# Kernel optimization log

Measured on AMD Instinct MI355X. Metric: run time of the kernel, lower is better.

The kernel has to match this reference:

```python
import jax, jax.numpy as jnp
import numpy as np

B, T, IN, H, OUT = 64, 2048, 64, 512, 32


def setup_inputs() -> dict:
    key = jax.random.key(0)
    ks = jax.random.split(key, 8)
    # xavier_normal with gain=0.5: std = gain * sqrt(2/(fan_in+fan_out))
    std_fz = 0.5 * np.sqrt(2.0 / ((IN + H) + 2 * H))
    std_r = 0.5 * np.sqrt(2.0 / ((IN + H) + H))
    # nn.Linear default init: uniform(-1/sqrt(fan_in), 1/sqrt(fan_in))
    lim = 1.0 / np.sqrt(H)
    return {
        "u": jax.random.normal(ks[0], (B, T, IN), dtype=jnp.float32),
        "x0": jax.random.uniform(ks[1], (B, 1, H), dtype=jnp.float32),
        "kernel_fz": std_fz * jax.random.normal(ks[2], (IN + H, 2 * H), dtype=jnp.float32),
        "bias_fz": jnp.zeros((2 * H,), dtype=jnp.float32),
        "kernel_r": std_r * jax.random.normal(ks[3], (IN + H, H), dtype=jnp.float32),
        "bias_r": jnp.zeros((H,), dtype=jnp.float32),
        "W_out": jax.random.uniform(ks[4], (OUT, H), dtype=jnp.float32, minval=-lim, maxval=lim),
        "b_out": jax.random.uniform(ks[5], (OUT,), dtype=jnp.float32, minval=-lim, maxval=lim),
    }


def reference(u, x0, kernel_fz, bias_fz, kernel_r, bias_r, W_out, b_out):
    Hd = kernel_r.shape[1]
    x_init = x0[:, 0, :]  # [B, H]

    def step(x, u_t):
        # u_t: [B, IN], x: [B, H]
        fz = jax.nn.sigmoid(jnp.concatenate([u_t, x], axis=-1) @ kernel_fz + bias_fz)
        f, z = fz[:, :Hd], fz[:, Hd:]
        r = jnp.tanh(jnp.concatenate([u_t, f * x], axis=-1) @ kernel_r + bias_r)
        xk = (1.0 - z) * x + z * r
        y = x @ W_out.T + b_out  # output computed from PREVIOUS state, as in torch step()
        return xk, y

    u_tb = jnp.swapaxes(u, 0, 1)  # [T, B, IN]
    _, ys = jax.lax.scan(step, x_init, u_tb)  # ys: [T, B, OUT]
    return jnp.swapaxes(ys, 0, 1)  # [B, T, OUT]
```

## Files before the change

kernel.cpp:

```cpp
#include <hip/hip_runtime.h>
#include <stdint.h>

#define B_    64
#define T_    2048
#define IN_   64
#define H_    512
#define H2_   1024
#define OUT_  32
#define KTOT  576

#define NBG   8
#define NCG   32
#define NTHR  256
#define BPG   8
#define KSL   18
#define RS    12

#define ABORT_IDX   0
#define CTR_OFF     1024
#define CTR_STRIDE  1024
#define NCTR        (NBG * 2)
#define BUF_BASE    (CTR_OFF + NCTR * CTR_STRIDE)
#define XSLAB       32768

__device__ __forceinline__ void gpubf(float* p, float v) {
  asm volatile("global_atomic_swap %0, %1, off sc1\n\ts_waitcnt vmcnt(0)"
               :: "v"(p), "v"(v) : "memory");
}
__device__ __forceinline__ void gaddu(unsigned* p, unsigned v) {
  asm volatile("global_atomic_add %0, %1, off sc1"
               :: "v"(p), "v"(v) : "memory");
}
__device__ __forceinline__ unsigned gpollu(const unsigned* p) {
  unsigned v;
  asm volatile("global_load_dword %0, %1, off sc0 sc1\n\ts_waitcnt vmcnt(0)"
               : "=v"(v) : "v"(p) : "memory");
  return v;
}
__device__ __forceinline__ void gload4x4(const float* p0, const float* p1,
                                         const float* p2, const float* p3,
                                         float4& a, float4& b, float4& c, float4& d) {
  asm volatile(
      "global_load_dwordx4 %0, %4, off sc0 sc1\n\t"
      "global_load_dwordx4 %1, %5, off sc0 sc1\n\t"
      "global_load_dwordx4 %2, %6, off sc0 sc1\n\t"
      "global_load_dwordx4 %3, %7, off sc0 sc1\n\t"
      "s_waitcnt vmcnt(0)"
      : "=&v"(a), "=&v"(b), "=&v"(c), "=&v"(d)
      : "v"(p0), "v"(p1), "v"(p2), "v"(p3)
      : "memory");
}

__global__ __launch_bounds__(256) void gru_init(float* ws, const float* __restrict__ x0) {
  int i = blockIdx.x * blockDim.x + threadIdx.x;
  int stride = gridDim.x * blockDim.x;
  unsigned* w = (unsigned*)ws;
  for (int k = i; k < BUF_BASE; k += stride) w[k] = 0u;
  for (int k = i; k < NBG * H_ * BPG; k += stride) {
    int bg = k >> 12, j = (k >> 3) & (H_ - 1), b = k & 7;
    ws[BUF_BASE + k] = x0[(bg * 8 + b) * H_ + j];
  }
}

__device__ __forceinline__ void gbar_arrive(unsigned* ctr) {
  __syncthreads();
  if (threadIdx.x == 0) gaddu(ctr, 1u);
}

__device__ __forceinline__ bool gbar_wait(unsigned* ctr, unsigned target,
                                          unsigned* abort_w) {
  __shared__ int s_ok;
  if (threadIdx.x == 0) {
    int ok = 1;
    int polls = 0;
    while (gpollu(ctr) < target) {
      __builtin_amdgcn_s_sleep(1);
      if ((++polls & 255) == 0) {
        if (__hip_atomic_load(abort_w, __ATOMIC_RELAXED, __HIP_MEMORY_SCOPE_AGENT) != 0u ||
            polls > 2000000) {
          __hip_atomic_store(abort_w, 1u, __ATOMIC_RELAXED, __HIP_MEMORY_SCOPE_AGENT);
          ok = 0;
          break;
        }
      }
    }
    s_ok = ok;
  }
  __syncthreads();
  __atomic_signal_fence(__ATOMIC_ACQUIRE);
  return s_ok != 0;
}

__global__ __launch_bounds__(NTHR, 1) void gru_main(
    const float* __restrict__ u, const float* __restrict__ kfz,
    const float* __restrict__ bfz, const float* __restrict__ kr,
    const float* __restrict__ br, const float* __restrict__ wout,
    const float* __restrict__ bout, float* __restrict__ out, float* ws) {
  unsigned* wsu = (unsigned*)ws;
  unsigned* abort_w = wsu + ABORT_IDX;
  float* xg0 = ws + BUF_BASE;
  float* xg1 = xg0 + XSLAB;
  float* xfg = xg1 + XSLAB;

  const int bg  = blockIdx.x & 7;
  const int cg  = blockIdx.x >> 3;
  const int tid = threadIdx.x;
  const int w   = tid >> 6;
  const int l   = tid & 63;
  const int cq  = l & 7;
  const int g   = l >> 3;
  const int kb  = (w * 8 + g) * KSL;
  const int fc  = tid >> 3;
  const int fb  = tid & 7;
  const int yb  = tid >> 5;
  const int yq  = tid & 31;

  unsigned* ctrA = wsu + CTR_OFF + (bg * 2 + 0) * CTR_STRIDE;
  unsigned* ctrB = wsu + CTR_OFF + (bg * 2 + 1) * CTR_STRIDE;

  __shared__ float bufA[KTOT * RS];
  __shared__ float pA[4 * 32 * RS];
  __shared__ float pB[4 * 16 * RS];
  __shared__ float rbuf[16 * 8];

  float wA[KSL][4];
#pragma unroll
  for (int i = 0; i < KSL; ++i)
#pragma unroll
    for (int m = 0; m < 4; ++m) {
      int c = 4 * cq + m;
      int gcol = (c < 16) ? (16 * cg + c) : (512 + 16 * cg + (c - 16));
      wA[i][m] = kfz[(size_t)(kb + i) * H2_ + gcol];
    }
  float wB[KSL][2];
#pragma unroll
  for (int i = 0; i < KSL; ++i)
#pragma unroll
    for (int m = 0; m < 2; ++m)
      wB[i][m] = kr[(size_t)(kb + i) * H_ + (16 * cg + 2 * cq + m)];
  float wy[16];
#pragma unroll
  for (int i = 0; i < 16; ++i) wy[i] = wout[cg * H_ + (yq + 32 * i)];
  const float by = bout[cg];
  const int fzc = (fc < 16) ? (16 * cg + fc) : (512 + 16 * cg + (fc - 16));
  const float biasA = bfz[fzc];
  const float biasB = (tid < 128) ? br[16 * cg + fc] : 0.0f;

  float zreg = 0.0f, xoldz = 0.0f;

  {
    int k2 = tid & 31, b = tid >> 5;
    float2 uv = *(const float2*)&u[((size_t)(bg * 8 + b) * T_) * IN_ + 2 * k2];
    bufA[(2 * k2) * RS + b] = uv.x;
    bufA[(2 * k2 + 1) * RS + b] = uv.y;
  }

  for (int t = 0; t < T_; ++t) {
    float* xcur = (t & 1) ? xg1 : xg0;
    float* xnxt = (t & 1) ? xg0 : xg1;

    {
      const float* s0 = &xcur[(size_t)(bg * H_ + tid) * 8];
      const float* s2 = &xcur[(size_t)(bg * H_ + tid + 256) * 8];
      float4 a, b, c, d;
      gload4x4(s0, s0 + 4, s2, s2 + 4, a, b, c, d);
      *(float4*)&bufA[(64 + tid) * RS] = a;
      *(float4*)&bufA[(64 + tid) * RS + 4] = b;
      *(float4*)&bufA[(64 + tid + 256) * RS] = c;
      *(float4*)&bufA[(64 + tid + 256) * RS + 4] = d;
    }
    __syncthreads();

    float acc[4][8] = {};
#pragma unroll
    for (int i = 0; i < KSL; ++i) {
      const float* xr = &bufA[(kb + i) * RS];
      float4 x0 = *(const float4*)xr;
      float4 x1 = *(const float4*)(xr + 4);
#pragma unroll
      for (int m = 0; m < 4; ++m) {
        float wv = wA[i][m];
        acc[m][0] += wv * x0.x; acc[m][1] += wv * x0.y;
        acc[m][2] += wv * x0.z; acc[m][3] += wv * x0.w;
        acc[m][4] += wv * x1.x; acc[m][5] += wv * x1.y;
        acc[m][6] += wv * x1.z; acc[m][7] += wv * x1.w;
      }
    }

#pragma unroll
    for (int m = 0; m < 4; ++m)
#pragma unroll
      for (int b = 0; b < 8; ++b) {
        acc[m][b] += __shfl_xor(acc[m][b], 8);
        acc[m][b] += __shfl_xor(acc[m][b], 16);
        acc[m][b] += __shfl_xor(acc[m][b], 32);
      }
    if (g == 0) {
#pragma unroll
      for (int m = 0; m < 4; ++m) {
        float* p = &pA[(w * 32 + 4 * cq + m) * RS];
        *(float4*)p = make_float4(acc[m][0], acc[m][1], acc[m][2], acc[m][3]);
        *(float4*)(p + 4) = make_float4(acc[m][4], acc[m][5], acc[m][6], acc[m][7]);
      }
    }
    __syncthreads();

    {
      float s = pA[(0 * 32 + fc) * RS + fb] + pA[(1 * 32 + fc) * RS + fb] +
                pA[(2 * 32 + fc) * RS + fb] + pA[(3 * 32 + fc) * RS + fb] + biasA;
      float sig = 1.0f / (1.0f + __expf(-s));
      if (fc < 16) {
        float xo = bufA[(64 + 16 * cg + fc) * RS + fb];
        gpubf(&xfg[(size_t)(bg * H_ + 16 * cg + fc) * 8 + fb], sig * xo);
      } else {
        zreg = sig;
        xoldz = bufA[(64 + 16 * cg + (fc - 16)) * RS + fb];
      }
    }

    gbar_arrive(ctrA);

    {
      float yp = 0.0f;
#pragma unroll
      for (int i = 0; i < 16; ++i)
        yp += wy[i] * bufA[(64 + yq + 32 * i) * RS + yb];
      yp += __shfl_xor(yp, 1);  yp += __shfl_xor(yp, 2);
      yp += __shfl_xor(yp, 4);  yp += __shfl_xor(yp, 8);
      yp += __shfl_xor(yp, 16);
      if (yq == 0)
        out[((size_t)(bg * 8 + yb) * T_ + t) * OUT_ + cg] = yp + by;
    }

    if (!gbar_wait(ctrA, (unsigned)(NCG * (t + 1)), abort_w)) return;

    {
      const float* s0 = &xfg[(size_t)(bg * H_ + tid) * 8];
      const float* s2 = &xfg[(size_t)(bg * H_ + tid + 256) * 8];
      float4 a, b, c, d;
      gload4x4(s0, s0 + 4, s2, s2 + 4, a, b, c, d);
      *(float4*)&bufA[(64 + tid) * RS] = a;
      *(float4*)&bufA[(64 + tid) * RS + 4] = b;
      *(float4*)&bufA[(64 + tid + 256) * RS] = c;
      *(float4*)&bufA[(64 + tid + 256) * RS + 4] = d;
    }
    __syncthreads();

    float acc2[2][8] = {};
#pragma unroll
    for (int i = 0; i < KSL; ++i) {
      const float* xr = &bufA[(kb + i) * RS];
      float4 x0 = *(const float4*)xr;
      float4 x1 = *(const float4*)(xr + 4);
#pragma unroll
      for (int m = 0; m < 2; ++m) {
        float wv = wB[i][m];
        acc2[m][0] += wv * x0.x; acc2[m][1] += wv * x0.y;
        acc2[m][2] += wv * x0.z; acc2[m][3] += wv * x0.w;
        acc2[m][4] += wv * x1.x; acc2[m][5] += wv * x1.y;
        acc2[m][6] += wv * x1.z; acc2[m][7] += wv * x1.w;
      }
    }
#pragma unroll
    for (int m = 0; m < 2; ++m)
#pragma unroll
      for (int b = 0; b < 8; ++b) {
        acc2[m][b] += __shfl_xor(acc2[m][b], 8);
        acc2[m][b] += __shfl_xor(acc2[m][b], 16);
        acc2[m][b] += __shfl_xor(acc2[m][b], 32);
      }
    if (g == 0) {
#pragma unroll
      for (int m = 0; m < 2; ++m) {
        float* p = &pB[(w * 16 + 2 * cq + m) * RS];
        *(float4*)p = make_float4(acc2[m][0], acc2[m][1], acc2[m][2], acc2[m][3]);
        *(float4*)(p + 4) = make_float4(acc2[m][4], acc2[m][5], acc2[m][6], acc2[m][7]);
      }
    }
    __syncthreads();

    if (tid < 128) {
      float s = pB[(0 * 16 + fc) * RS + fb] + pB[(1 * 16 + fc) * RS + fb] +
                pB[(2 * 16 + fc) * RS + fb] + pB[(3 * 16 + fc) * RS + fb] + biasB;
      float e = __expf(2.0f * s);
      rbuf[fc * 8 + fb] = 1.0f - 2.0f / (1.0f + e);
    }
    __syncthreads();

    if (tid >= 128) {
      float r = rbuf[(fc - 16) * 8 + fb];
      float xn = xoldz + zreg * (r - xoldz);
      gpubf(&xnxt[(size_t)(bg * H_ + 16 * cg + (fc - 16)) * 8 + fb], xn);
    }

    gbar_arrive(ctrB);

    if (t + 1 < T_) {
      int k2 = tid & 31, b = tid >> 5;
      float2 uv = *(const float2*)&u[((size_t)(bg * 8 + b) * T_ + (t + 1)) * IN_ + 2 * k2];
      bufA[(2 * k2) * RS + b] = uv.x;
      bufA[(2 * k2 + 1) * RS + b] = uv.y;
    }

    if (!gbar_wait(ctrB, (unsigned)(NCG * (t + 1)), abort_w)) return;
  }
}

extern "C" void kernel_launch(void* const* d_in, const int* in_sizes, int n_in,
                              void* d_out, int out_size, void* d_ws, size_t ws_size,
                              hipStream_t stream) {
  const float* u    = (const float*)d_in[0];
  const float* x0   = (const float*)d_in[1];
  const float* kfz  = (const float*)d_in[2];
  const float* bfz  = (const float*)d_in[3];
  const float* kr   = (const float*)d_in[4];
  const float* br   = (const float*)d_in[5];
  const float* wout = (const float*)d_in[6];
  const float* bout = (const float*)d_in[7];
  float* out = (float*)d_out;
  float* ws  = (float*)d_ws;

  hipLaunchKernelGGL(gru_init, dim3(64), dim3(256), 0, stream, ws, x0);
  hipLaunchKernelGGL(gru_main, dim3(NBG * NCG), dim3(NTHR), 0, stream,
                     u, kfz, bfz, kr, br, wout, bout, out, ws);
}
```

Measured before the change: 13.93 ms.

## Merge column-group pairs into 512-thread blocks to halve grid-barrier participants

Each block now handles two column groups with two 256-thread halves, so the grid shrinks from 256 to 128 blocks and each barrier waits on half as many arrivals. The two halves share the staged state buffer in LDS, so each block loads the state slab once instead of twice. Publishes use 64-bit atomic swaps of two batch values with a single waitcnt before arrival, replacing per-element swaps that each waited. The cost is heavier per-block register and LDS use and fewer active CUs, which may lengthen each step's compute.

```diff
diff --git a/kernel.cpp b/kernel.cpp
--- a/kernel.cpp
+++ b/kernel.cpp
@@ -10,8 +10,8 @@
 #define KTOT  576
 
 #define NBG   8
-#define NCG   32
-#define NTHR  256
+#define NCGH  16
+#define NTHR  512
 #define BPG   8
 #define KSL   18
 #define RS    12
@@ -23,9 +23,12 @@
 #define BUF_BASE    (CTR_OFF + NCTR * CTR_STRIDE)
 #define XSLAB       32768
 
-__device__ __forceinline__ void gpubf(float* p, float v) {
-  asm volatile("global_atomic_swap %0, %1, off sc1\n\ts_waitcnt vmcnt(0)"
-               :: "v"(p), "v"(v) : "memory");
+__device__ __forceinline__ void gpub2f(float* p, float v0, float v1) {
+  unsigned long long q =
+      ((unsigned long long)__float_as_uint(v1) << 32) |
+      (unsigned long long)__float_as_uint(v0);
+  asm volatile("global_atomic_swap_x2 %0, %1, off sc1"
+               :: "v"(p), "v"(q) : "memory");
 }
 __device__ __forceinline__ void gaddu(unsigned* p, unsigned v) {
   asm volatile("global_atomic_add %0, %1, off sc1"
@@ -37,17 +40,14 @@
                : "=v"(v) : "v"(p) : "memory");
   return v;
 }
-__device__ __forceinline__ void gload4x4(const float* p0, const float* p1,
-                                         const float* p2, const float* p3,
-                                         float4& a, float4& b, float4& c, float4& d) {
+__device__ __forceinline__ void gload2(const float* p0, const float* p1,
+                                       float4& a, float4& b) {
   asm volatile(
-      "global_load_dwordx4 %0, %4, off sc0 sc1\n\t"
-      "global_load_dwordx4 %1, %5, off sc0 sc1\n\t"
-      "global_load_dwordx4 %2, %6, off sc0 sc1\n\t"
-      "global_load_dwordx4 %3, %7, off sc0 sc1\n\t"
+      "global_load_dwordx4 %0, %2, off sc0 sc1\n\t"
+      "global_load_dwordx4 %1, %3, off sc0 sc1\n\t"
       "s_waitcnt vmcnt(0)"
-      : "=&v"(a), "=&v"(b), "=&v"(c), "=&v"(d)
-      : "v"(p0), "v"(p1), "v"(p2), "v"(p3)
+      : "=&v"(a), "=&v"(b)
+      : "v"(p0), "v"(p1)
       : "memory");
 }
 
@@ -60,11 +60,6 @@
     int bg = k >> 12, j = (k >> 3) & (H_ - 1), b = k & 7;
     ws[BUF_BASE + k] = x0[(bg * 8 + b) * H_ + j];
   }
-}
-
-__device__ __forceinline__ void gbar_arrive(unsigned* ctr) {
-  __syncthreads();
-  if (threadIdx.x == 0) gaddu(ctr, 1u);
 }
 
 __device__ __forceinline__ bool gbar_wait(unsigned* ctr, unsigned target,
@@ -102,26 +97,34 @@
   float* xg1 = xg0 + XSLAB;
   float* xfg = xg1 + XSLAB;
 
-  const int bg  = blockIdx.x & 7;
-  const int cg  = blockIdx.x >> 3;
-  const int tid = threadIdx.x;
-  const int w   = tid >> 6;
-  const int l   = tid & 63;
-  const int cq  = l & 7;
-  const int g   = l >> 3;
-  const int kb  = (w * 8 + g) * KSL;
-  const int fc  = tid >> 3;
-  const int fb  = tid & 7;
-  const int yb  = tid >> 5;
-  const int yq  = tid & 31;
+  const int bg   = blockIdx.x & 7;
+  const int cgh  = blockIdx.x >> 3;
+  const int tid  = threadIdx.x;
+  const int sub  = tid >> 8;
+  const int vtid = tid & 255;
+  const int vcg  = cgh * 2 + sub;
+  const int w    = vtid >> 6;
+  const int l    = vtid & 63;
+  const int cq   = l & 7;
+  const int g    = l >> 3;
+  const int kb   = (w * 8 + g) * KSL;
+  const int prow = (vtid & 127) >> 2;
+  const int b0   = (vtid & 3) * 2;
+  const int fcB  = vtid >> 3;
+  const int fbB  = vtid & 7;
+  const int yb   = vtid >> 5;
+  const int yq   = vtid & 31;
 
   unsigned* ctrA = wsu + CTR_OFF + (bg * 2 + 0) * CTR_STRIDE;
   unsigned* ctrB = wsu + CTR_OFF + (bg * 2 + 1) * CTR_STRIDE;
 
   __shared__ float bufA[KTOT * RS];
-  __shared__ float pA[4 * 32 * RS];
-  __shared__ float pB[4 * 16 * RS];
-  __shared__ float rbuf[16 * 8];
+  __shared__ float pA[2][4 * 32 * RS];
+  __shared__ float pB[2][4 * 16 * RS];
+  __shared__ float rbuf[2][16 * 8];
+  float* pAs = pA[sub];
+  float* pBs = pB[sub];
+  float* rbs = rbuf[sub];
 
   float wA[KSL][4];
 #pragma unroll
@@ -129,7 +132,7 @@
 #pragma unroll
     for (int m = 0; m < 4; ++m) {
       int c = 4 * cq + m;
-      int gcol = (c < 16) ? (16 * cg + c) : (512 + 16 * cg + (c - 16));
+      int gcol = (c < 16) ? (16 * vcg + c) : (512 + 16 * vcg + (c - 16));
       wA[i][m] = kfz[(size_t)(kb + i) * H2_ + gcol];
     }
   float wB[KSL][2];
@@ -137,18 +140,18 @@
   for (int i = 0; i < KSL; ++i)
 #pragma unroll
     for (int m = 0; m < 2; ++m)
-      wB[i][m] = kr[(size_t)(kb + i) * H_ + (16 * cg + 2 * cq + m)];
+      wB[i][m] = kr[(size_t)(kb + i) * H_ + (16 * vcg + 2 * cq + m)];
   float wy[16];
 #pragma unroll
-  for (int i = 0; i < 16; ++i) wy[i] = wout[cg * H_ + (yq + 32 * i)];
-  const float by = bout[cg];
-  const int fzc = (fc < 16) ? (16 * cg + fc) : (512 + 16 * cg + (fc - 16));
-  const float biasA = bfz[fzc];
-  const float biasB = (tid < 128) ? br[16 * cg + fc] : 0.0f;
-
-  float zreg = 0.0f, xoldz = 0.0f;
-
-  {
+  for (int i = 0; i < 16; ++i) wy[i] = wout[vcg * H_ + (yq + 32 * i)];
+  const float by = bout[vcg];
+  const int fzc = (prow < 16) ? (16 * vcg + prow) : (512 + 16 * vcg + (prow - 16));
+  const float biasA = ((vtid & 255) < 128) ? bfz[fzc] : 0.0f;
+  const float biasB = (vtid < 128) ? br[16 * vcg + fcB] : 0.0f;
+
+  float zreg0 = 0.0f, zreg1 = 0.0f, xoldz0 = 0.0f, xoldz1 = 0.0f;
+
+  if (tid < 256) {
     int k2 = tid & 31, b = tid >> 5;
     float2 uv = *(const float2*)&u[((size_t)(bg * 8 + b) * T_) * IN_ + 2 * k2];
     bufA[(2 * k2) * RS + b] = uv.x;
@@ -161,13 +164,10 @@
 
     {
       const float* s0 = &xcur[(size_t)(bg * H_ + tid) * 8];
-      const float* s2 = &xcur[(size_t)(bg * H_ + tid + 256) * 8];
-      float4 a, b, c, d;
-      gload4x4(s0, s0 + 4, s2, s2 + 4, a, b, c, d);
+      float4 a, b;
+      gload2(s0, s0 + 4, a, b);
       *(float4*)&bufA[(64 + tid) * RS] = a;
       *(float4*)&bufA[(64 + tid) * RS + 4] = b;
-      *(float4*)&bufA[(64 + tid + 256) * RS] = c;
-      *(float4*)&bufA[(64 + tid + 256) * RS + 4] = d;
     }
     __syncthreads();
 
@@ -198,51 +198,58 @@
     if (g == 0) {
 #pragma unroll
       for (int m = 0; m < 4; ++m) {
-        float* p = &pA[(w * 32 + 4 * cq + m) * RS];
+        float* p = &pAs[(w * 32 + 4 * cq + m) * RS];
         *(float4*)p = make_float4(acc[m][0], acc[m][1], acc[m][2], acc[m][3]);
         *(float4*)(p + 4) = make_float4(acc[m][4], acc[m][5], acc[m][6], acc[m][7]);
       }
     }
     __syncthreads();
 
+    if (vtid < 128) {
+      float s0 = pAs[(0 * 32 + prow) * RS + b0] + pAs[(1 * 32 + prow) * RS + b0] +
+                 pAs[(2 * 32 + prow) * RS + b0] + pAs[(3 * 32 + prow) * RS + b0] + biasA;
+      float s1 = pAs[(0 * 32 + prow) * RS + b0 + 1] + pAs[(1 * 32 + prow) * RS + b0 + 1] +
+                 pAs[(2 * 32 + prow) * RS + b0 + 1] + pAs[(3 * 32 + prow) * RS + b0 + 1] + biasA;
+      float sig0 = 1.0f / (1.0f + __expf(-s0));
+      float sig1 = 1.0f / (1.0f + __expf(-s1));
+      if (prow < 16) {
+        int col = 16 * vcg + prow;
+        float xo0 = bufA[(64 + col) * RS + b0];
+        float xo1 = bufA[(64 + col) * RS + b0 + 1];
+        gpub2f(&xfg[((size_t)bg * H_ + col) * 8 + b0], sig0 * xo0, sig1 * xo1);
+      } else {
+        int col = 16 * vcg + (prow - 16);
+        zreg0 = sig0; zreg1 = sig1;
+        xoldz0 = bufA[(64 + col) * RS + b0];
+        xoldz1 = bufA[(64 + col) * RS + b0 + 1];
+      }
+    }
+
+    float yp = 0.0f;
     {
-      float s = pA[(0 * 32 + fc) * RS + fb] + pA[(1 * 32 + fc) * RS + fb] +
-                pA[(2 * 32 + fc) * RS + fb] + pA[(3 * 32 + fc) * RS + fb] + biasA;
-      float sig = 1.0f / (1.0f + __expf(-s));
-      if (fc < 16) {
-        float xo = bufA[(64 + 16 * cg + fc) * RS + fb];
-        gpubf(&xfg[(size_t)(bg * H_ + 16 * cg + fc) * 8 + fb], sig * xo);
-      } else {
-        zreg = sig;
-        xoldz = bufA[(64 + 16 * cg + (fc - 16)) * RS + fb];
-      }
-    }
-
-    gbar_arrive(ctrA);
-
-    {
-      float yp = 0.0f;
 #pragma unroll
       for (int i = 0; i < 16; ++i)
         yp += wy[i] * bufA[(64 + yq + 32 * i) * RS + yb];
       yp += __shfl_xor(yp, 1);  yp += __shfl_xor(yp, 2);
       yp += __shfl_xor(yp, 4);  yp += __shfl_xor(yp, 8);
       yp += __shfl_xor(yp, 16);
-      if (yq == 0)
-        out[((size_t)(bg * 8 + yb) * T_ + t) * OUT_ + cg] = yp + by;
-    }
-
-    if (!gbar_wait(ctrA, (unsigned)(NCG * (t + 1)), abort_w)) return;
+    }
+
+    asm volatile("s_waitcnt vmcnt(0)" ::: "memory");
+    __syncthreads();
+    if (tid == 0) gaddu(ctrA, 1u);
+
+    if (yq == 0)
+      out[((size_t)(bg * 8 + yb) * T_ + t) * OUT_ + vcg] = yp + by;
+
+    if (!gbar_wait(ctrA, (unsigned)(NCGH * (t + 1)), abort_w)) return;
 
     {
       const float* s0 = &xfg[(size_t)(bg * H_ + tid) * 8];
-      const float* s2 = &xfg[(size_t)(bg * H_ + tid + 256) * 8];
-      float4 a, b, c, d;
-      gload4x4(s0, s0 + 4, s2, s2 + 4, a, b, c, d);
+      float4 a, b;
+      gload2(s0, s0 + 4, a, b);
       *(float4*)&bufA[(64 + tid) * RS] = a;
       *(float4*)&bufA[(64 + tid) * RS + 4] = b;
-      *(float4*)&bufA[(64 + tid + 256) * RS] = c;
-      *(float4*)&bufA[(64 + tid + 256) * RS + 4] = d;
     }
     __syncthreads();
 
@@ -272,37 +279,42 @@
     if (g == 0) {
 #pragma unroll
       for (int m = 0; m < 2; ++m) {
-        float* p = &pB[(w * 16 + 2 * cq + m) * RS];
+        float* p = &pBs[(w * 16 + 2 * cq + m) * RS];
         *(float4*)p = make_float4(acc2[m][0], acc2[m][1], acc2[m][2], acc2[m][3]);
         *(float4*)(p + 4) = make_float4(acc2[m][4], acc2[m][5], acc2[m][6], acc2[m][7]);
       }
     }
     __syncthreads();
 
-    if (tid < 128) {
-      float s = pB[(0 * 16 + fc) * RS + fb] + pB[(1 * 16 + fc) * RS + fb] +
-                pB[(2 * 16 + fc) * RS + fb] + pB[(3 * 16 + fc) * RS + fb] + biasB;
+    if (vtid < 128) {
+      float s = pBs[(0 * 16 + fcB) * RS + fbB] + pBs[(1 * 16 + fcB) * RS + fbB] +
+                pBs[(2 * 16 + fcB) * RS + fbB] + pBs[(3 * 16 + fcB) * RS + fbB] + biasB;
       float e = __expf(2.0f * s);
-      rbuf[fc * 8 + fb] = 1.0f - 2.0f / (1.0f + e);
-    }
-    __syncthreads();
-
-    if (tid >= 128) {
-      float r = rbuf[(fc - 16) * 8 + fb];
-      float xn = xoldz + zreg * (r - xoldz);
-      gpubf(&xnxt[(size_t)(bg * H_ + 16 * cg + (fc - 16)) * 8 + fb], xn);
-    }
-
-    gbar_arrive(ctrB);
-
-    if (t + 1 < T_) {
+      rbs[fcB * 8 + fbB] = 1.0f - 2.0f / (1.0f + e);
+    }
+    __syncthreads();
+
+    if (vtid >= 64 && vtid < 128) {
+      int zr = prow - 16;
+      float r0 = rbs[zr * 8 + b0];
+      float r1 = rbs[zr * 8 + b0 + 1];
+      float xn0 = xoldz0 + zreg0 * (r0 - xoldz0);
+      float xn1 = xoldz1 + zreg1 * (r1 - xoldz1);
+      gpub2f(&xnxt[((size_t)bg * H_ + 16 * vcg + zr) * 8 + b0], xn0, xn1);
+    }
+
+    if (tid < 256 && t + 1 < T_) {
       int k2 = tid & 31, b = tid >> 5;
       float2 uv = *(const float2*)&u[((size_t)(bg * 8 + b) * T_ + (t + 1)) * IN_ + 2 * k2];
       bufA[(2 * k2) * RS + b] = uv.x;
       bufA[(2 * k2 + 1) * RS + b] = uv.y;
     }
 
-    if (!gbar_wait(ctrB, (unsigned)(NCG * (t + 1)), abort_w)) return;
+    asm volatile("s_waitcnt vmcnt(0)" ::: "memory");
+    __syncthreads();
+    if (tid == 0) gaddu(ctrB, 1u);
+
+    if (!gbar_wait(ctrB, (unsigned)(NCGH * (t + 1)), abort_w)) return;
   }
 }
 
@@ -321,6 +333,6 @@
   float* ws  = (float*)d_ws;
 
   hipLaunchKernelGGL(gru_init, dim3(64), dim3(256), 0, stream, ws, x0);
-  hipLaunchKernelGGL(gru_main, dim3(NBG * NCG), dim3(NTHR), 0, stream,
+  hipLaunchKernelGGL(gru_main, dim3(NBG * NCGH), dim3(NTHR), 0, stream,
                      u, kfz, bfz, kr, br, wout, bout, out, ws);
 }
```

Result: slower. 38.67 ms (+177.7%).

## Pack state publishes into 64-bit atomic swaps and defer waitcnt to barrier

Applied to the files above, without the earlier changes.

Each thread now publishes two batch elements with a single global_atomic_swap_x2 instead of one 32-bit swap per element, halving the number of cross-block atomic stores. The per-store s_waitcnt is dropped and replaced by a single waitcnt before the barrier arrive. The y output projection is moved ahead of the arrive and its store moved after it, so the barrier signal and the publishes overlap with other work. This relies on the 8-byte alignment of the paired slots and on the single waitcnt still ordering the publishes before the counter increment.

```diff
diff --git a/kernel.cpp b/kernel.cpp
--- a/kernel.cpp
+++ b/kernel.cpp
@@ -23,9 +23,12 @@
 #define BUF_BASE    (CTR_OFF + NCTR * CTR_STRIDE)
 #define XSLAB       32768
 
-__device__ __forceinline__ void gpubf(float* p, float v) {
-  asm volatile("global_atomic_swap %0, %1, off sc1\n\ts_waitcnt vmcnt(0)"
-               :: "v"(p), "v"(v) : "memory");
+__device__ __forceinline__ void gpub2f(float* p, float v0, float v1) {
+  unsigned long long q =
+      ((unsigned long long)__float_as_uint(v1) << 32) |
+      (unsigned long long)__float_as_uint(v0);
+  asm volatile("global_atomic_swap_x2 %0, %1, off sc1"
+               :: "v"(p), "v"(q) : "memory");
 }
 __device__ __forceinline__ void gaddu(unsigned* p, unsigned v) {
   asm volatile("global_atomic_add %0, %1, off sc1"
@@ -60,11 +63,6 @@
     int bg = k >> 12, j = (k >> 3) & (H_ - 1), b = k & 7;
     ws[BUF_BASE + k] = x0[(bg * 8 + b) * H_ + j];
   }
-}
-
-__device__ __forceinline__ void gbar_arrive(unsigned* ctr) {
-  __syncthreads();
-  if (threadIdx.x == 0) gaddu(ctr, 1u);
 }
 
 __device__ __forceinline__ bool gbar_wait(unsigned* ctr, unsigned target,
@@ -110,6 +108,8 @@
   const int cq  = l & 7;
   const int g   = l >> 3;
   const int kb  = (w * 8 + g) * KSL;
+  const int prow = tid >> 2;
+  const int pb0  = (tid & 3) * 2;
   const int fc  = tid >> 3;
   const int fb  = tid & 7;
   const int yb  = tid >> 5;
@@ -142,11 +142,11 @@
 #pragma unroll
   for (int i = 0; i < 16; ++i) wy[i] = wout[cg * H_ + (yq + 32 * i)];
   const float by = bout[cg];
-  const int fzc = (fc < 16) ? (16 * cg + fc) : (512 + 16 * cg + (fc - 16));
-  const float biasA = bfz[fzc];
+  const int fzc = (prow < 16) ? (16 * cg + prow) : (512 + 16 * cg + (prow - 16));
+  const float biasA = (tid < 128) ? bfz[fzc] : 0.0f;
   const float biasB = (tid < 128) ? br[16 * cg + fc] : 0.0f;
 
-  float zreg = 0.0f, xoldz = 0.0f;
+  float zreg0 = 0.0f, zreg1 = 0.0f, xoldz0 = 0.0f, xoldz1 = 0.0f;
 
   {
     int k2 = tid & 31, b = tid >> 5;
@@ -205,32 +205,42 @@
     }
     __syncthreads();
 
+    if (tid < 128) {
+      float s0 = pA[(0 * 32 + prow) * RS + pb0] + pA[(1 * 32 + prow) * RS + pb0] +
+                 pA[(2 * 32 + prow) * RS + pb0] + pA[(3 * 32 + prow) * RS + pb0] + biasA;
+      float s1 = pA[(0 * 32 + prow) * RS + pb0 + 1] + pA[(1 * 32 + prow) * RS + pb0 + 1] +
+                 pA[(2 * 32 + prow) * RS + pb0 + 1] + pA[(3 * 32 + prow) * RS + pb0 + 1] + biasA;
+      float sig0 = 1.0f / (1.0f + __expf(-s0));
+      float sig1 = 1.0f / (1.0f + __expf(-s1));
+      if (prow < 16) {
+        int col = 16 * cg + prow;
+        float xo0 = bufA[(64 + col) * RS + pb0];
+        float xo1 = bufA[(64 + col) * RS + pb0 + 1];
+        gpub2f(&xfg[((size_t)bg * H_ + col) * 8 + pb0], sig0 * xo0, sig1 * xo1);
+      } else {
+        int col = 16 * cg + (prow - 16);
+        zreg0 = sig0; zreg1 = sig1;
+        xoldz0 = bufA[(64 + col) * RS + pb0];
+        xoldz1 = bufA[(64 + col) * RS + pb0 + 1];
+      }
+    }
+
+    float yp = 0.0f;
     {
-      float s = pA[(0 * 32 + fc) * RS + fb] + pA[(1 * 32 + fc) * RS + fb] +
-                pA[(2 * 32 + fc) * RS + fb] + pA[(3 * 32 + fc) * RS + fb] + biasA;
-      float sig = 1.0f / (1.0f + __expf(-s));
-      if (fc < 16) {
-        float xo = bufA[(64 + 16 * cg + fc) * RS + fb];
-        gpubf(&xfg[(size_t)(bg * H_ + 16 * cg + fc) * 8 + fb], sig * xo);
-      } else {
-        zreg = sig;
-        xoldz = bufA[(64 + 16 * cg + (fc - 16)) * RS + fb];
-      }
-    }
-
-    gbar_arrive(ctrA);
-
-    {
-      float yp = 0.0f;
 #pragma unroll
       for (int i = 0; i < 16; ++i)
         yp += wy[i] * bufA[(64 + yq + 32 * i) * RS + yb];
       yp += __shfl_xor(yp, 1);  yp += __shfl_xor(yp, 2);
       yp += __shfl_xor(yp, 4);  yp += __shfl_xor(yp, 8);
       yp += __shfl_xor(yp, 16);
-      if (yq == 0)
-        out[((size_t)(bg * 8 + yb) * T_ + t) * OUT_ + cg] = yp + by;
-    }
+    }
+
+    asm volatile("s_waitcnt vmcnt(0)" ::: "memory");
+    __syncthreads();
+    if (tid == 0) gaddu(ctrA, 1u);
+
+    if (yq == 0)
+      out[((size_t)(bg * 8 + yb) * T_ + t) * OUT_ + cg] = yp + by;
 
     if (!gbar_wait(ctrA, (unsigned)(NCG * (t + 1)), abort_w)) return;
 
@@ -287,13 +297,14 @@
     }
     __syncthreads();
 
-    if (tid >= 128) {
-      float r = rbuf[(fc - 16) * 8 + fb];
-      float xn = xoldz + zreg * (r - xoldz);
-      gpubf(&xnxt[(size_t)(bg * H_ + 16 * cg + (fc - 16)) * 8 + fb], xn);
-    }
-
-    gbar_arrive(ctrB);
+    if (tid >= 64 && tid < 128) {
+      int zr = prow - 16;
+      float r0 = rbuf[zr * 8 + pb0];
+      float r1 = rbuf[zr * 8 + pb0 + 1];
+      float xn0 = xoldz0 + zreg0 * (r0 - xoldz0);
+      float xn1 = xoldz1 + zreg1 * (r1 - xoldz1);
+      gpub2f(&xnxt[((size_t)bg * H_ + 16 * cg + zr) * 8 + pb0], xn0, xn1);
+    }
 
     if (t + 1 < T_) {
       int k2 = tid & 31, b = tid >> 5;
@@ -301,6 +312,10 @@
       bufA[(2 * k2) * RS + b] = uv.x;
       bufA[(2 * k2 + 1) * RS + b] = uv.y;
     }
+
+    asm volatile("s_waitcnt vmcnt(0)" ::: "memory");
+    __syncthreads();
+    if (tid == 0) gaddu(ctrB, 1u);
 
     if (!gbar_wait(ctrB, (unsigned)(NCG * (t + 1)), abort_w)) return;
   }
```

New measurement: 15.61 ms. 12.1% more time.
